# Kernel optimization log

Measured on AMD Instinct MI355X. Metric: run time of the kernel, lower is better.

## Reference

```python
import jax, jax.numpy as jnp
import numpy as np

B, S, D, H = 2, 2048, 1024, 16
HD = D // H  # head_size = 64


def setup_inputs() -> dict:
    key = jax.random.key(0)
    ks = jax.random.split(key, 11)
    s = 1.0 / np.sqrt(D)
    inp = {
        "q": jax.random.normal(ks[0], (B, S, D), jnp.float32),
        "k": jax.random.normal(ks[1], (B, S, D), jnp.float32),
        "v": jax.random.normal(ks[2], (B, S, D), jnp.float32),
        "Wq": jax.random.normal(ks[3], (D, D), jnp.float32) * s,
        "bq": jax.random.normal(ks[4], (D,), jnp.float32) * s,
        "Wk": jax.random.normal(ks[5], (D, D), jnp.float32) * s,
        "bk": jax.random.normal(ks[6], (D,), jnp.float32) * s,
        "Wv": jax.random.normal(ks[7], (D, D), jnp.float32) * s,
        "bv": jax.random.normal(ks[8], (D,), jnp.float32) * s,
        "Wo": jax.random.normal(ks[9], (D, D), jnp.float32) * s,
        "bo": jax.random.normal(ks[10], (D,), jnp.float32) * s,
    }
    return inp


def reference(q, k, v, Wq, bq, Wk, bk, Wv, bv, Wo, bo):
    # project and split heads: [B,S,D] -> [B,H,S,HD]
    def split_heads(x, W, b):
        y = x @ W.T + b
        return y.reshape(B, S, H, HD).transpose(0, 2, 1, 3)

    qh = split_heads(q, Wq, bq)
    kh = split_heads(k, Wk, bk)
    vh = split_heads(v, Wv, bv)

    scale = 1.0 / jnp.sqrt(jnp.asarray(HD, qh.dtype))
    scores = jnp.einsum("bhqd,bhkd->bhqk", qh, kh) * scale  # [B,H,S,S]
    weights = jax.nn.softmax(scores, axis=-1)
    out = jnp.einsum("bhqk,bhkd->bhqd", weights, vh)  # [B,H,S,HD]
    out = out.transpose(0, 2, 1, 3).reshape(B, S, D)
    return out @ Wo.T + bo
```

## Files before the change

### kernel.cpp

```cpp
#include <hip/hip_runtime.h>

typedef __attribute__((ext_vector_type(4))) float f32x4;
typedef __attribute__((ext_vector_type(8))) short bf16x8;
typedef __attribute__((ext_vector_type(8))) unsigned short u16x8;
typedef __attribute__((ext_vector_type(4))) unsigned short u16x4;
typedef __attribute__((ext_vector_type(4))) unsigned int u32x4;
typedef unsigned short ushort_t;

#define LOG2E 1.4426950408889634f

__device__ inline unsigned short f2bf(float x) {
  union { float f; unsigned int u; } v; v.f = x;
  unsigned int r = v.u + 0x7fffu + ((v.u >> 16) & 1u);
  return (unsigned short)(r >> 16);
}

__device__ inline unsigned cvtpk_bf16(float a, float b) {
  unsigned r;
  asm("v_cvt_pk_bf16_f32 %0, %1, %2" : "=v"(r) : "v"(a), "v"(b));
  return r;
}

__device__ inline void gload_lds16(const void* g, void* l) {
  __builtin_amdgcn_global_load_lds(
      (const __attribute__((address_space(1))) unsigned int*)g,
      (__attribute__((address_space(3))) unsigned int*)l, 16, 0, 0);
}

__device__ inline void cvt_body(const float* __restrict__ src, ushort_t* __restrict__ dst, int i) {
  const f32x4* s = (const f32x4*)src;
  f32x4 a = s[2 * i], b = s[2 * i + 1];
  u16x8 o;
#pragma unroll
  for (int j = 0; j < 4; ++j) { o[j] = f2bf(a[j]); o[4 + j] = f2bf(b[j]); }
  *(u16x8*)(dst + (size_t)i * 8) = o;
}

__global__ __launch_bounds__(256) void cvt_bf16(const float* __restrict__ src,
                                                ushort_t* __restrict__ dst, int n8) {
  int i = blockIdx.x * 256 + threadIdx.x;
  if (i < n8) cvt_body(src, dst, i);
}

__global__ __launch_bounds__(256) void cvt_all(const float* __restrict__ q,
                                               const float* __restrict__ k,
                                               const float* __restrict__ v,
                                               const float* __restrict__ Wq,
                                               const float* __restrict__ Wk,
                                               const float* __restrict__ Wv,
                                               const float* __restrict__ Wo,
                                               ushort_t* __restrict__ Xb,
                                               ushort_t* __restrict__ Wb, int nx8) {
  int i = blockIdx.x * 256 + threadIdx.x;
  int z = blockIdx.y;
  if (z < 3) {
    if (i < nx8) cvt_body(z == 0 ? q : (z == 1 ? k : v), Xb + (size_t)z * nx8 * 8, i);
  } else {
    int w = i >> 17, off = i & 131071;
    const float* s = w == 0 ? Wq : (w == 1 ? Wk : (w == 2 ? Wv : Wo));
    cvt_body(s, Wb + (size_t)w * 1048576, off);
  }
}

template <typename F>
__device__ inline void gemm_core32(const ushort_t* __restrict__ A, const ushort_t* __restrict__ W,
                                   int m0, int n0,
                                   ushort_t (&As)[2][128 * 32], ushort_t (&Bs)[2][128 * 32],
                                   F&& mfma_step) {
  constexpr int K = 1024;
  const int tid = threadIdx.x, lane = tid & 63, wid = tid >> 6;
  const int srow = lane >> 2, sp = lane & 3;
  const int sOffLane = srow * 1024 + (sp ^ ((srow >> 1) & 3)) * 8;

  const ushort_t* aR = A + (size_t)m0 * K;
  const ushort_t* wR = W + (size_t)n0 * K;

  auto stage = [&](const ushort_t* aSrc, const ushort_t* wSrc, int db) {
#pragma unroll
    for (int c = 0; c < 2; ++c) {
      int i = wid * 2 + c;
      gload_lds16(aSrc + (size_t)i * 16384 + sOffLane, &As[db][i * 512]);
      gload_lds16(wSrc + (size_t)i * 16384 + sOffLane, &Bs[db][i * 512]);
    }
  };

  stage(aR, wR, 0);
  aR += 32; wR += 32;
  __syncthreads();
  for (int k0 = 0; k0 < K; k0 += 32) {
    const int buf = (k0 >> 5) & 1;
    if (k0 + 32 < K) {
      stage(aR, wR, buf ^ 1);
      aR += 32; wR += 32;
    }
    mfma_step(As[buf], Bs[buf]);
    __syncthreads();
  }
}

__global__ __launch_bounds__(256) void proj_gemm(const ushort_t* __restrict__ Abase, int aStride,
                                                 const ushort_t* __restrict__ Wall, int wStride,
                                                 const float* __restrict__ bq,
                                                 const float* __restrict__ bk,
                                                 const float* __restrict__ bv, float qs,
                                                 ushort_t* __restrict__ outQ,
                                                 ushort_t* __restrict__ outK,
                                                 ushort_t* __restrict__ outV, int zofs) {
  __shared__ __attribute__((aligned(16))) ushort_t As[2][128 * 32];
  __shared__ __attribute__((aligned(16))) ushort_t Bs[2][128 * 32];
  const int z = blockIdx.z + zofs;
  const ushort_t* A = Abase + (size_t)z * aStride;
  const ushort_t* W = Wall + (size_t)z * wStride;
  const float* bias = z == 0 ? bq : (z == 1 ? bk : bv);
  const float scale = z == 0 ? qs : 1.0f;
  ushort_t* out = z == 0 ? outQ : (z == 1 ? outK : outV);
  const int mode = z == 2 ? 1 : 0;

  const int tid = threadIdx.x, lane = tid & 63, wid = tid >> 6;
  const int m0 = blockIdx.x * 128, n0 = blockIdx.y * 128;
  const int wm = wid >> 1, wn = wid & 1;
  const int qr = lane & 15, kq = lane >> 4;
  const int rOff = qr * 32 + ((kq ^ ((qr >> 1) & 3)) * 8);
  const int aOff = wm * 2048 + rOff, bOff = wn * 2048 + rOff;
  f32x4 acc[4][4] = {};

  gemm_core32(A, W, m0, n0, As, Bs, [&](ushort_t* as, ushort_t* bs) {
    bf16x8 a[4], b[4];
#pragma unroll
    for (int f = 0; f < 4; ++f) {
      a[f] = *(const bf16x8*)(as + aOff + f * 512);
      b[f] = *(const bf16x8*)(bs + bOff + f * 512);
    }
#pragma unroll
    for (int i = 0; i < 4; ++i)
#pragma unroll
      for (int j = 0; j < 4; ++j)
        acc[i][j] = __builtin_amdgcn_mfma_f32_16x16x32_bf16(a[i], b[j], acc[i][j], 0, 0, 0);
  });

  const int cm = m0 + wm * 64, cn = n0 + wn * 64;
#pragma unroll
  for (int fn = 0; fn < 4; ++fn) {
    int n = cn + fn * 16 + qr;
    float bvv = bias[n];
    int h = n >> 6, hd = n & 63;
#pragma unroll
    for (int fm = 0; fm < 4; ++fm) {
      int m = cm + fm * 16 + kq * 4;
      if (mode == 0) {
#pragma unroll
        for (int r = 0; r < 4; ++r) {
          int mm = m + r, b = mm >> 11, s = mm & 2047;
          out[((size_t)(b * 16 + h) * 2048 + s) * 64 + hd] = f2bf((acc[fm][fn][r] + bvv) * scale);
        }
      } else {
        int b = m >> 11, s = m & 2047;
        u16x4 pk;
#pragma unroll
        for (int r = 0; r < 4; ++r) pk[r] = f2bf((acc[fm][fn][r] + bvv) * scale);
        *(u16x4*)&out[((size_t)(b * 16 + h) * 64 + hd) * 2048 + s] = pk;
      }
    }
  }
}

__global__ __launch_bounds__(256) void gemm_out(const ushort_t* __restrict__ A,
                                                const ushort_t* __restrict__ W,
                                                const float* __restrict__ bias,
                                                float* __restrict__ out) {
  __shared__ __attribute__((aligned(16))) ushort_t As[2][128 * 32];
  __shared__ __attribute__((aligned(16))) ushort_t Bs[2][128 * 32];
  const int tid = threadIdx.x, lane = tid & 63, wid = tid >> 6;
  const int m0 = blockIdx.x * 128, n0 = blockIdx.y * 128;
  const int wm = wid >> 1, wn = wid & 1;
  const int qr = lane & 15, kq = lane >> 4;
  const int rOff = qr * 32 + ((kq ^ ((qr >> 1) & 3)) * 8);
  const int aOff = wm * 2048 + rOff, bOff = wn * 2048 + rOff;
  f32x4 acc[4][4] = {};

  gemm_core32(A, W, m0, n0, As, Bs, [&](ushort_t* as, ushort_t* bs) {
    bf16x8 a[4], b[4];
#pragma unroll
    for (int f = 0; f < 4; ++f) {
      a[f] = *(const bf16x8*)(as + aOff + f * 512);
      b[f] = *(const bf16x8*)(bs + bOff + f * 512);
    }
#pragma unroll
    for (int i = 0; i < 4; ++i)
#pragma unroll
      for (int j = 0; j < 4; ++j)
        acc[i][j] = __builtin_amdgcn_mfma_f32_16x16x32_bf16(a[i], b[j], acc[i][j], 0, 0, 0);
  });

  const int cm = m0 + wm * 64, cn = n0 + wn * 64;
#pragma unroll
  for (int fn = 0; fn < 4; ++fn) {
    int n = cn + fn * 16 + qr;
    float bvv = bias[n];
#pragma unroll
    for (int fm = 0; fm < 4; ++fm) {
      int m = cm + fm * 16 + kq * 4;
#pragma unroll
      for (int r = 0; r < 4; ++r) out[(size_t)(m + r) * 1024 + n] = acc[fm][fn][r] + bvv;
    }
  }
}

__global__ __launch_bounds__(256) void attn_fwd(const ushort_t* __restrict__ Qh,
                                                const ushort_t* __restrict__ Kh,
                                                const ushort_t* __restrict__ Vt,
                                                ushort_t* __restrict__ ctx) {
  constexpr int S = 2048, HD = 64, NT = S / 64;
  __shared__ __attribute__((aligned(16))) ushort_t Ks[2][64 * 64];
  __shared__ __attribute__((aligned(16))) ushort_t Vs[2][64 * 64];

  const int tid = threadIdx.x, lane = tid & 63, wid = tid >> 6;
  const int bh = blockIdx.y, qt = blockIdx.x;
  const size_t head = (size_t)bh * S * HD;
  const ushort_t* Qp = Qh + head;
  const ushort_t* Kp = Kh + head;
  const ushort_t* Vp = Vt + head;

  const int qr = lane & 15, kq = lane >> 4;
  const int q0 = qt * 64 + wid * 16;

  bf16x8 qf[2];
  qf[0] = *(const bf16x8*)&Qp[(size_t)(q0 + qr) * HD + kq * 8];
  qf[1] = *(const bf16x8*)&Qp[(size_t)(q0 + qr) * HD + 32 + kq * 8];

  f32x4 accO[4] = {};
  float mrun = -3e38f, lrun = 0.f;

  const int srow8 = lane >> 3, sp8 = lane & 7;
  const int qr7 = qr & 7;
  const int offA = qr * 64 + ((kq ^ qr7) * 8);
  const int offB = qr * 64 + (((4 + kq) ^ qr7) * 8);
  const int kStageOff = srow8 * 64 + ((sp8 ^ srow8) * 8);
  const int vStageOff = srow8 * 2048 + ((sp8 ^ srow8) * 8);

  auto stageK = [&](const ushort_t* src, ushort_t* dst) {
#pragma unroll
    for (int c = 0; c < 2; ++c) {
      int i = wid * 2 + c;
      gload_lds16(src + (size_t)i * 512 + kStageOff, dst + i * 512);
    }
  };
  auto stageV = [&](const ushort_t* src, ushort_t* dst) {
#pragma unroll
    for (int c = 0; c < 2; ++c) {
      int i = wid * 2 + c;
      gload_lds16(src + (size_t)i * 16384 + vStageOff, dst + i * 512);
    }
  };

  stageK(Kp, Ks[0]);
  stageV(Vp, Vs[0]);
  __syncthreads();
  stageK(Kp + 4096, Ks[1]);
  stageV(Vp + 64, Vs[1]);
  const ushort_t* kR = Kp + 8192;
  const ushort_t* vR = Vp + 128;

  for (int t = 0; t < NT; ++t) {
    const int buf = t & 1;
    if (t >= 1 && t + 1 < NT) {
      stageK(kR, Ks[buf ^ 1]);
      stageV(vR, Vs[buf ^ 1]);
      kR += 4096;
      vR += 64;
    }

    const ushort_t* kb = Ks[buf];
    f32x4 sc[4] = {};
    __builtin_amdgcn_s_setprio(1);
#pragma unroll
    for (int fn = 0; fn < 4; ++fn) {
      bf16x8 kf0 = *(const bf16x8*)(kb + offA + fn * 1024);
      sc[fn] = __builtin_amdgcn_mfma_f32_16x16x32_bf16(kf0, qf[0], sc[fn], 0, 0, 0);
      bf16x8 kf1 = *(const bf16x8*)(kb + offB + fn * 1024);
      sc[fn] = __builtin_amdgcn_mfma_f32_16x16x32_bf16(kf1, qf[1], sc[fn], 0, 0, 0);
    }
    __builtin_amdgcn_s_setprio(0);

    float t0 = fmaxf(fmaxf(fmaxf(sc[0][0], sc[0][1]), sc[0][2]), sc[0][3]);
    float t1 = fmaxf(fmaxf(fmaxf(sc[1][0], sc[1][1]), sc[1][2]), sc[1][3]);
    float t2 = fmaxf(fmaxf(fmaxf(sc[2][0], sc[2][1]), sc[2][2]), sc[2][3]);
    float t3 = fmaxf(fmaxf(fmaxf(sc[3][0], sc[3][1]), sc[3][2]), sc[3][3]);
    float pm = fmaxf(fmaxf(t0, t1), fmaxf(t2, t3));
    pm = fmaxf(pm, __shfl_xor(pm, 16, 64));
    pm = fmaxf(pm, __shfl_xor(pm, 32, 64));

    bool need = pm > mrun + 8.0f;
    if (__any(need)) {
      float mn = need ? pm : mrun;
      float sf = __builtin_amdgcn_exp2f(mrun - mn);
      mrun = mn;
#pragma unroll
      for (int f2 = 0; f2 < 4; ++f2) accO[f2] *= sf;
      lrun *= sf;
    }

    float pv[4][4];
    float sum = 0.f;
#pragma unroll
    for (int fn = 0; fn < 4; ++fn)
#pragma unroll
      for (int r = 0; r < 4; ++r) {
        float p = __builtin_amdgcn_exp2f(sc[fn][r] - mrun);
        pv[fn][r] = p;
        sum += p;
      }
    sum += __shfl_xor(sum, 16, 64);
    sum += __shfl_xor(sum, 32, 64);
    lrun += sum;

    unsigned wv[4][2];
#pragma unroll
    for (int fn = 0; fn < 4; ++fn) {
      wv[fn][0] = cvtpk_bf16(pv[fn][0], pv[fn][1]);
      wv[fn][1] = cvtpk_bf16(pv[fn][2], pv[fn][3]);
    }

    const ushort_t* vb = Vs[buf];
    __builtin_amdgcn_s_setprio(1);
#pragma unroll
    for (int ks = 0; ks < 2; ++ks) {
      unsigned a0 = wv[2 * ks][0], b0 = wv[2 * ks + 1][0];
      unsigned a1 = wv[2 * ks][1], b1 = wv[2 * ks + 1][1];
      asm volatile("v_permlane32_swap_b32 %0, %1" : "+v"(a0), "+v"(b0));
      asm volatile("v_permlane16_swap_b32 %0, %1" : "+v"(a0), "+v"(b0));
      asm volatile("v_permlane32_swap_b32 %0, %1" : "+v"(a1), "+v"(b1));
      asm volatile("v_permlane16_swap_b32 %0, %1" : "+v"(a1), "+v"(b1));
      u32x4 praw;
      praw[0] = a0; praw[1] = a1; praw[2] = b0; praw[3] = b1;
      bf16x8 pf = __builtin_bit_cast(bf16x8, praw);
      const int vOff = ks == 0 ? offA : offB;
#pragma unroll
      for (int f2 = 0; f2 < 4; ++f2) {
        bf16x8 vf = *(const bf16x8*)(vb + vOff + f2 * 1024);
        accO[f2] = __builtin_amdgcn_mfma_f32_16x16x32_bf16(vf, pf, accO[f2], 0, 0, 0);
      }
    }
    __builtin_amdgcn_s_setprio(0);
    __syncthreads();
  }

  float inv = 1.0f / lrun;
  const int b = bh >> 4, h = bh & 15;
#pragma unroll
  for (int f2 = 0; f2 < 4; ++f2) {
    u16x4 pk;
#pragma unroll
    for (int r = 0; r < 4; ++r) pk[r] = f2bf(accO[f2][r] * inv);
    int col = h * 64 + f2 * 16 + kq * 4;
    *(u16x4*)&ctx[((size_t)b * 2048 + q0 + qr) * 1024 + col] = pk;
  }
}

extern "C" void kernel_launch(void* const* d_in, const int* in_sizes, int n_in,
                              void* d_out, int out_size, void* d_ws, size_t ws_size,
                              hipStream_t stream) {
  const float* q = (const float*)d_in[0];
  const float* k = (const float*)d_in[1];
  const float* v = (const float*)d_in[2];
  const float* Wq = (const float*)d_in[3];
  const float* bq = (const float*)d_in[4];
  const float* Wk = (const float*)d_in[5];
  const float* bk = (const float*)d_in[6];
  const float* Wv = (const float*)d_in[7];
  const float* bv = (const float*)d_in[8];
  const float* Wo = (const float*)d_in[9];
  const float* bo = (const float*)d_in[10];

  char* ws = (char*)d_ws;
  const size_t MB = 1024 * 1024;
  const int NXE = 4194304;
  const int NWE = 1048576;
  const float qs = 0.125f * LOG2E;
  dim3 gg(32, 8), ga(32, 32);

  if (ws_size >= 56 * MB) {
    ushort_t* Xb = (ushort_t*)(ws);
    ushort_t* Wb = (ushort_t*)(ws + 24 * MB);
    ushort_t* Qh = (ushort_t*)(ws + 32 * MB);
    ushort_t* Kh = (ushort_t*)(ws + 40 * MB);
    ushort_t* Vt = (ushort_t*)(ws + 48 * MB);
    cvt_all<<<dim3(2048, 4), 256, 0, stream>>>(q, k, v, Wq, Wk, Wv, Wo, Xb, Wb, NXE / 8);
    proj_gemm<<<dim3(32, 8, 3), 256, 0, stream>>>(Xb, NXE, Wb, NWE, bq, bk, bv, qs,
                                                  Qh, Kh, Vt, 0);
    attn_fwd<<<ga, 256, 0, stream>>>(Qh, Kh, Vt, Xb);
    gemm_out<<<gg, 256, 0, stream>>>(Xb, Wb + (size_t)3 * NWE, bo, (float*)d_out);
  } else if (ws_size >= 40 * MB) {
    ushort_t* Xb = (ushort_t*)(ws);
    ushort_t* Wb = (ushort_t*)(ws + 8 * MB);
    ushort_t* Qh = (ushort_t*)(ws + 16 * MB);
    ushort_t* Kh = (ushort_t*)(ws + 24 * MB);
    ushort_t* Vt = (ushort_t*)(ws + 32 * MB);
    const float* xs[3] = {q, k, v};
    for (int z = 0; z < 3; ++z) {
      cvt_bf16<<<2048, 256, 0, stream>>>(xs[z], Xb, NXE / 8);
      if (z == 0)
        cvt_all<<<dim3(2048, 1), 256, 0, stream>>>(q, k, v, Wq, Wk, Wv, Wo, Xb, Wb, 0);
      proj_gemm<<<dim3(32, 8, 1), 256, 0, stream>>>(Xb, 0, Wb, NWE, bq, bk, bv, qs,
                                                    Qh, Kh, Vt, z);
    }
    attn_fwd<<<ga, 256, 0, stream>>>(Qh, Kh, Vt, Xb);
    gemm_out<<<gg, 256, 0, stream>>>(Xb, Wb + (size_t)3 * NWE, bo, (float*)d_out);
  } else {
    ushort_t* Xb = (ushort_t*)(ws);
    ushort_t* Wb = (ushort_t*)(ws + 8 * MB);
    ushort_t* Qh = (ushort_t*)(ws + 10 * MB);
    ushort_t* Kh = (ushort_t*)(ws + 18 * MB);
    ushort_t* Vt = (ushort_t*)(ws + 26 * MB);
    const float* xs[3] = {q, k, v};
    const float* wsrc[3] = {Wq, Wk, Wv};
    for (int z = 0; z < 3; ++z) {
      cvt_bf16<<<2048, 256, 0, stream>>>(xs[z], Xb, NXE / 8);
      cvt_bf16<<<512, 256, 0, stream>>>(wsrc[z], Wb, NWE / 8);
      proj_gemm<<<dim3(32, 8, 1), 256, 0, stream>>>(Xb, 0, Wb, 0, bq, bk, bv, qs,
                                                    Qh, Kh, Vt, z);
    }
    attn_fwd<<<ga, 256, 0, stream>>>(Qh, Kh, Vt, Xb);
    cvt_bf16<<<512, 256, 0, stream>>>(Wo, Wb, NWE / 8);
    gemm_out<<<gg, 256, 0, stream>>>(Xb, Wb, bo, (float*)d_out);
  }
}
```

Before: 141.8 us.

## Fuse fp32-to-bf16 activation conversion into projection GEMM A-tile loading

The projection GEMM now reads fp32 q/k/v directly into registers, converts them to bf16 with packed cvt instructions, and writes them into shared memory. This removes the separate activation conversion pass and its bf16 staging buffer. Only the weights are still converted, by a smaller cvt4 kernel. The cost is more global read traffic per GEMM tile (fp32 A reads repeated across the 8 N-tiles) and a register round-trip in place of direct global-to-LDS loads for A.

After: 153.0 us. 7.9% more time.

```diff
diff --git a/kernel.cpp b/kernel.cpp
--- a/kernel.cpp
+++ b/kernel.cpp
@@ -42,24 +42,15 @@
   if (i < n8) cvt_body(src, dst, i);
 }
 
-__global__ __launch_bounds__(256) void cvt_all(const float* __restrict__ q,
-                                               const float* __restrict__ k,
-                                               const float* __restrict__ v,
-                                               const float* __restrict__ Wq,
-                                               const float* __restrict__ Wk,
-                                               const float* __restrict__ Wv,
-                                               const float* __restrict__ Wo,
-                                               ushort_t* __restrict__ Xb,
-                                               ushort_t* __restrict__ Wb, int nx8) {
+__global__ __launch_bounds__(256) void cvt4(const float* __restrict__ Wq,
+                                            const float* __restrict__ Wk,
+                                            const float* __restrict__ Wv,
+                                            const float* __restrict__ Wo,
+                                            ushort_t* __restrict__ Wb) {
   int i = blockIdx.x * 256 + threadIdx.x;
   int z = blockIdx.y;
-  if (z < 3) {
-    if (i < nx8) cvt_body(z == 0 ? q : (z == 1 ? k : v), Xb + (size_t)z * nx8 * 8, i);
-  } else {
-    int w = i >> 17, off = i & 131071;
-    const float* s = w == 0 ? Wq : (w == 1 ? Wk : (w == 2 ? Wv : Wo));
-    cvt_body(s, Wb + (size_t)w * 1048576, off);
-  }
+  const float* s = z == 0 ? Wq : (z == 1 ? Wk : (z == 2 ? Wv : Wo));
+  cvt_body(s, Wb + (size_t)z * 1048576, i);
 }
 
 template <typename F>
@@ -98,7 +89,75 @@
   }
 }
 
-__global__ __launch_bounds__(256) void proj_gemm(const ushort_t* __restrict__ Abase, int aStride,
+template <typename F>
+__device__ inline void gemm_core32_f32A(const float* __restrict__ Af,
+                                        const ushort_t* __restrict__ W,
+                                        int m0, int n0,
+                                        ushort_t (&As)[2][128 * 32],
+                                        ushort_t (&Bs)[2][128 * 32],
+                                        F&& mfma_step) {
+  constexpr int K = 1024;
+  const int tid = threadIdx.x, lane = tid & 63, wid = tid >> 6;
+  const int srow = lane >> 2, sp = lane & 3;
+  const int sOffLane = srow * 1024 + (sp ^ ((srow >> 1) & 3)) * 8;
+
+  const float* aR = Af + (size_t)m0 * K;
+  const ushort_t* wR = W + (size_t)n0 * K;
+
+  f32x4 ra[2][2];
+
+  auto loadA = [&](const float* aSrc) {
+#pragma unroll
+    for (int c = 0; c < 2; ++c) {
+      int i = wid * 2 + c;
+      const float* p = aSrc + (size_t)i * 16384 + sOffLane;
+      ra[c][0] = *(const f32x4*)(p);
+      ra[c][1] = *(const f32x4*)(p + 4);
+    }
+  };
+  auto writeA = [&](int db) {
+#pragma unroll
+    for (int c = 0; c < 2; ++c) {
+      int i = wid * 2 + c;
+      u32x4 w;
+      w[0] = cvtpk_bf16(ra[c][0][0], ra[c][0][1]);
+      w[1] = cvtpk_bf16(ra[c][0][2], ra[c][0][3]);
+      w[2] = cvtpk_bf16(ra[c][1][0], ra[c][1][1]);
+      w[3] = cvtpk_bf16(ra[c][1][2], ra[c][1][3]);
+      *(u32x4*)&As[db][i * 512 + lane * 8] = w;
+    }
+  };
+  auto stageW = [&](const ushort_t* wSrc, int db) {
+#pragma unroll
+    for (int c = 0; c < 2; ++c) {
+      int i = wid * 2 + c;
+      gload_lds16(wSrc + (size_t)i * 16384 + sOffLane, &Bs[db][i * 512]);
+    }
+  };
+
+  loadA(aR);
+  stageW(wR, 0);
+  writeA(0);
+  aR += 32; wR += 32;
+  __syncthreads();
+
+  for (int k0 = 0; k0 < K; k0 += 32) {
+    const int buf = (k0 >> 5) & 1;
+    const bool more = k0 + 32 < K;
+    if (more) {
+      loadA(aR);
+      stageW(wR, buf ^ 1);
+      aR += 32; wR += 32;
+    }
+    mfma_step(As[buf], Bs[buf]);
+    if (more) writeA(buf ^ 1);
+    __syncthreads();
+  }
+}
+
+__global__ __launch_bounds__(256) void proj_gemm(const float* __restrict__ qf,
+                                                 const float* __restrict__ kf,
+                                                 const float* __restrict__ vf,
                                                  const ushort_t* __restrict__ Wall, int wStride,
                                                  const float* __restrict__ bq,
                                                  const float* __restrict__ bk,
@@ -109,7 +168,7 @@
   __shared__ __attribute__((aligned(16))) ushort_t As[2][128 * 32];
   __shared__ __attribute__((aligned(16))) ushort_t Bs[2][128 * 32];
   const int z = blockIdx.z + zofs;
-  const ushort_t* A = Abase + (size_t)z * aStride;
+  const float* A = z == 0 ? qf : (z == 1 ? kf : vf);
   const ushort_t* W = Wall + (size_t)z * wStride;
   const float* bias = z == 0 ? bq : (z == 1 ? bk : bv);
   const float scale = z == 0 ? qs : 1.0f;
@@ -124,7 +183,7 @@
   const int aOff = wm * 2048 + rOff, bOff = wn * 2048 + rOff;
   f32x4 acc[4][4] = {};
 
-  gemm_core32(A, W, m0, n0, As, Bs, [&](ushort_t* as, ushort_t* bs) {
+  gemm_core32_f32A(A, W, m0, n0, As, Bs, [&](ushort_t* as, ushort_t* bs) {
     bf16x8 a[4], b[4];
 #pragma unroll
     for (int f = 0; f < 4; ++f) {
@@ -374,36 +433,19 @@
 
   char* ws = (char*)d_ws;
   const size_t MB = 1024 * 1024;
-  const int NXE = 4194304;
   const int NWE = 1048576;
   const float qs = 0.125f * LOG2E;
   dim3 gg(32, 8), ga(32, 32);
 
-  if (ws_size >= 56 * MB) {
-    ushort_t* Xb = (ushort_t*)(ws);
-    ushort_t* Wb = (ushort_t*)(ws + 24 * MB);
-    ushort_t* Qh = (ushort_t*)(ws + 32 * MB);
-    ushort_t* Kh = (ushort_t*)(ws + 40 * MB);
-    ushort_t* Vt = (ushort_t*)(ws + 48 * MB);
-    cvt_all<<<dim3(2048, 4), 256, 0, stream>>>(q, k, v, Wq, Wk, Wv, Wo, Xb, Wb, NXE / 8);
-    proj_gemm<<<dim3(32, 8, 3), 256, 0, stream>>>(Xb, NXE, Wb, NWE, bq, bk, bv, qs,
-                                                  Qh, Kh, Vt, 0);
-    attn_fwd<<<ga, 256, 0, stream>>>(Qh, Kh, Vt, Xb);
-    gemm_out<<<gg, 256, 0, stream>>>(Xb, Wb + (size_t)3 * NWE, bo, (float*)d_out);
-  } else if (ws_size >= 40 * MB) {
+  if (ws_size >= 40 * MB) {
     ushort_t* Xb = (ushort_t*)(ws);
     ushort_t* Wb = (ushort_t*)(ws + 8 * MB);
     ushort_t* Qh = (ushort_t*)(ws + 16 * MB);
     ushort_t* Kh = (ushort_t*)(ws + 24 * MB);
     ushort_t* Vt = (ushort_t*)(ws + 32 * MB);
-    const float* xs[3] = {q, k, v};
-    for (int z = 0; z < 3; ++z) {
-      cvt_bf16<<<2048, 256, 0, stream>>>(xs[z], Xb, NXE / 8);
-      if (z == 0)
-        cvt_all<<<dim3(2048, 1), 256, 0, stream>>>(q, k, v, Wq, Wk, Wv, Wo, Xb, Wb, 0);
-      proj_gemm<<<dim3(32, 8, 1), 256, 0, stream>>>(Xb, 0, Wb, NWE, bq, bk, bv, qs,
-                                                    Qh, Kh, Vt, z);
-    }
+    cvt4<<<dim3(512, 4), 256, 0, stream>>>(Wq, Wk, Wv, Wo, Wb);
+    proj_gemm<<<dim3(32, 8, 3), 256, 0, stream>>>(q, k, v, Wb, NWE, bq, bk, bv, qs,
+                                                  Qh, Kh, Vt, 0);
     attn_fwd<<<ga, 256, 0, stream>>>(Qh, Kh, Vt, Xb);
     gemm_out<<<gg, 256, 0, stream>>>(Xb, Wb + (size_t)3 * NWE, bo, (float*)d_out);
   } else {
@@ -412,12 +454,10 @@
     ushort_t* Qh = (ushort_t*)(ws + 10 * MB);
     ushort_t* Kh = (ushort_t*)(ws + 18 * MB);
     ushort_t* Vt = (ushort_t*)(ws + 26 * MB);
-    const float* xs[3] = {q, k, v};
     const float* wsrc[3] = {Wq, Wk, Wv};
     for (int z = 0; z < 3; ++z) {
-      cvt_bf16<<<2048, 256, 0, stream>>>(xs[z], Xb, NXE / 8);
       cvt_bf16<<<512, 256, 0, stream>>>(wsrc[z], Wb, NWE / 8);
-      proj_gemm<<<dim3(32, 8, 1), 256, 0, stream>>>(Xb, 0, Wb, 0, bq, bk, bv, qs,
+      proj_gemm<<<dim3(32, 8, 1), 256, 0, stream>>>(q, k, v, Wb, 0, bq, bk, bv, qs,
                                                     Qh, Kh, Vt, z);
     }
     attn_fwd<<<ga, 256, 0, stream>>>(Qh, Kh, Vt, Xb);
```
